# Performance work log

Measured on AMD Instinct MI355X. Metric: run time of the kernel, lower is better.

Reference implementation:

```python
import jax, jax.numpy as jnp
import numpy as np

N_NODES = 100000


def _gcn_norm(edge_src, edge_dst, n):
    ones = jnp.ones(edge_src.shape[0], dtype=jnp.float32)
    deg_out = jax.ops.segment_sum(ones, edge_src, num_segments=n)
    deg_in = jax.ops.segment_sum(ones, edge_dst, num_segments=n)
    norm_src = jax.lax.rsqrt(jnp.maximum(deg_out, 1.0))
    norm_dst = jax.lax.rsqrt(jnp.maximum(deg_in, 1.0))
    return norm_src, norm_dst


def _graph_conv(h, edge_src, edge_dst, norm_src, norm_dst, W, b, act):
    # symmetric-normalized aggregation: D^-1/2 A D^-1/2 h, then linear
    m = (h * norm_src[:, None])[edge_src]                       # [E, d] gather
    agg = jax.ops.segment_sum(m, edge_dst, num_segments=h.shape[0])  # [N, d] scatter-add
    agg = agg * norm_dst[:, None]
    out = agg @ W + b[: W.shape[1]]
    return act(out) if act is not None else out


def setup_inputs() -> dict:
    key = jax.random.key(0)
    ks = jax.random.split(key, 8)
    d_in, d_h, n_cls, E = 64, 64, 40, 1000000
    return {
        "features": jax.random.normal(ks[0], (N_NODES, d_in), dtype=jnp.float32),
        "edge_src": jax.random.randint(ks[1], (E,), 0, N_NODES),
        "edge_dst": jax.random.randint(ks[2], (E,), 0, N_NODES),
        "W1": jax.random.normal(ks[3], (d_in, d_h), dtype=jnp.float32) * (1.0 / np.sqrt(d_in)),
        "b1": jnp.zeros((d_h,), dtype=jnp.float32),
        "W2": jax.random.normal(ks[4], (d_h, d_h), dtype=jnp.float32) * (1.0 / np.sqrt(d_h)),
        "b2": jnp.zeros((d_h,), dtype=jnp.float32),
        "W3": jax.random.normal(ks[5], (d_h, n_cls), dtype=jnp.float32) * (1.0 / np.sqrt(d_h)),
        "b3": jnp.zeros((d_h,), dtype=jnp.float32),
    }


def reference(features, edge_src, edge_dst, W1, b1, W2, b2, W3, b3):
    norm_src, norm_dst = _gcn_norm(edge_src, edge_dst, features.shape[0])
    h = _graph_conv(features, edge_src, edge_dst, norm_src, norm_dst, W1, b1, jax.nn.relu)
    h = _graph_conv(h, edge_src, edge_dst, norm_src, norm_dst, W2, b2, jax.nn.relu)
    h = _graph_conv(h, edge_src, edge_dst, norm_src, norm_dst, W3, b3, None)
    return h
```

## Files before the change

kernel.cpp:

```cpp
#include <hip/hip_runtime.h>
#include <hip/hip_fp16.h>

#define D 64
#define THREADS 256
#define CAP 40
#define BSTRIDE 44

__global__ void init_kernel(int* __restrict__ cnt_out, int* __restrict__ buckets, int n) {
    int i = blockIdx.x * blockDim.x + threadIdx.x;
    if (i < n) {
        cnt_out[i] = 0;
        buckets[(size_t)i * BSTRIDE] = 0;
    }
}

__global__ void build_kernel(const int* __restrict__ src, const int* __restrict__ dst,
                             int* __restrict__ cnt_out, int* __restrict__ buckets, int E) {
    int base = (blockIdx.x * blockDim.x + threadIdx.x) * 4;
    if (base + 3 < E) {
        int4 s4 = *(const int4*)(src + base);
        int4 d4 = *(const int4*)(dst + base);
        atomicAdd(&cnt_out[s4.x], 1);
        atomicAdd(&cnt_out[s4.y], 1);
        atomicAdd(&cnt_out[s4.z], 1);
        atomicAdd(&cnt_out[s4.w], 1);
        int p0 = atomicAdd(&buckets[(size_t)d4.x * BSTRIDE], 1);
        int p1 = atomicAdd(&buckets[(size_t)d4.y * BSTRIDE], 1);
        int p2 = atomicAdd(&buckets[(size_t)d4.z * BSTRIDE], 1);
        int p3 = atomicAdd(&buckets[(size_t)d4.w * BSTRIDE], 1);
        if (p0 < CAP) buckets[(size_t)d4.x * BSTRIDE + 4 + p0] = s4.x;
        if (p1 < CAP) buckets[(size_t)d4.y * BSTRIDE + 4 + p1] = s4.y;
        if (p2 < CAP) buckets[(size_t)d4.z * BSTRIDE + 4 + p2] = s4.z;
        if (p3 < CAP) buckets[(size_t)d4.w * BSTRIDE + 4 + p3] = s4.w;
    } else {
        for (int i = base; i < E; ++i) {
            int s = src[i], d = dst[i];
            atomicAdd(&cnt_out[s], 1);
            int pos = atomicAdd(&buckets[(size_t)d * BSTRIDE], 1);
            if (pos < CAP) buckets[(size_t)d * BSTRIDE + 4 + pos] = s;
        }
    }
}

__global__ void prescale_kernel(const float* __restrict__ feat, const int* __restrict__ cnt_out,
                                __half* __restrict__ outp, int n16) {
    int i = blockIdx.x * blockDim.x + threadIdx.x;
    if (i < n16) {
        float s = rsqrtf(fmaxf((float)cnt_out[i >> 4], 1.0f));
        float4 v = ((const float4*)feat)[i];
        __half2 lo = __floats2half2_rn(v.x * s, v.y * s);
        __half2 hi = __floats2half2_rn(v.z * s, v.w * s);
        uint2 u;
        u.x = *(unsigned*)&lo;
        u.y = *(unsigned*)&hi;
        ((uint2*)outp)[i] = u;
    }
}

__device__ __forceinline__ float bcast(float v, int l) {
    return __uint_as_float(__builtin_amdgcn_readlane(__float_as_uint(v), l));
}

template <int DOUT, bool RELU, bool SOUT, bool OUT_HALF>
__global__ __launch_bounds__(THREADS)
void layer_kernel(const __half* __restrict__ h, const int* __restrict__ buckets,
                  const int* __restrict__ cnt_out,
                  const float* __restrict__ W, const float* __restrict__ b,
                  void* __restrict__ outv, int n) {
    const int t = threadIdx.x;
    const int wave = t >> 6;
    const int lane = t & 63;
    const int grp  = lane >> 4;
    const int c    = lane & 15;
    const int ln   = (lane < DOUT) ? lane : (DOUT - 1);

    float4 Wc[16];
#pragma unroll
    for (int k4 = 0; k4 < 16; ++k4) {
        Wc[k4].x = W[(4 * k4 + 0) * DOUT + ln];
        Wc[k4].y = W[(4 * k4 + 1) * DOUT + ln];
        Wc[k4].z = W[(4 * k4 + 2) * DOUT + ln];
        Wc[k4].w = W[(4 * k4 + 3) * DOUT + ln];
    }
    const float bl = b[ln];

    const int nquads = (n + 3) >> 2;
    for (int qd = blockIdx.x * 4 + wave; qd < nquads; qd += gridDim.x * 4) {
        int node0 = qd * 4;
        int node  = node0 + grp;
        bool valid = node < n;
        int node_c = valid ? node : 0;
        size_t bbase = (size_t)node_c * BSTRIDE;
        int dg = valid ? buckets[bbase] : 0;
        if (dg > CAP) dg = CAP;
        const int* epos = buckets + bbase + 4;

        float ax = 0.f, ay = 0.f, az = 0.f, aw = 0.f;
        float bx = 0.f, by = 0.f, bz = 0.f, bw = 0.f;

        int4 q0 = *(const int4*)(epos + 0);
        int4 q1 = *(const int4*)(epos + 4);
        int4 q2 = *(const int4*)(epos + 8);
        int4 q3 = *(const int4*)(epos + 12);
        int sidx[16];
        sidx[0]=q0.x; sidx[1]=q0.y; sidx[2]=q0.z; sidx[3]=q0.w;
        sidx[4]=q1.x; sidx[5]=q1.y; sidx[6]=q1.z; sidx[7]=q1.w;
        sidx[8]=q2.x; sidx[9]=q2.y; sidx[10]=q2.z; sidx[11]=q2.w;
        sidx[12]=q3.x; sidx[13]=q3.y; sidx[14]=q3.z; sidx[15]=q3.w;

        uint2 u[16];
#pragma unroll
        for (int j = 0; j < 16; ++j) {
            unsigned sj = (j < dg) ? (unsigned)sidx[j] : 0u;
            u[j] = *((const uint2*)(h + ((size_t)sj << 6)) + c);
        }
#pragma unroll
        for (int j = 0; j < 16; ++j) {
            float wj = (j < dg) ? 1.f : 0.f;
            float2 lo = __half22float2(*(__half2*)&u[j].x);
            float2 hi = __half22float2(*(__half2*)&u[j].y);
            if (j & 1) {
                ax = fmaf(lo.x, wj, ax); ay = fmaf(lo.y, wj, ay);
                az = fmaf(hi.x, wj, az); aw = fmaf(hi.y, wj, aw);
            } else {
                bx = fmaf(lo.x, wj, bx); by = fmaf(lo.y, wj, by);
                bz = fmaf(hi.x, wj, bz); bw = fmaf(hi.y, wj, bw);
            }
        }
        for (int e = 16; e < dg; e += 4) {
            int4 i4 = *(const int4*)(epos + e);
            int rem = dg - e;
            unsigned s0 = (unsigned)i4.x;
            unsigned s1 = (rem > 1) ? (unsigned)i4.y : 0u;
            unsigned s2 = (rem > 2) ? (unsigned)i4.z : 0u;
            unsigned s3 = (rem > 3) ? (unsigned)i4.w : 0u;
            float w1 = (rem > 1) ? 1.f : 0.f;
            float w2 = (rem > 2) ? 1.f : 0.f;
            float w3 = (rem > 3) ? 1.f : 0.f;
            uint2 u0 = *((const uint2*)(h + ((size_t)s0 << 6)) + c);
            uint2 u1 = *((const uint2*)(h + ((size_t)s1 << 6)) + c);
            uint2 u2 = *((const uint2*)(h + ((size_t)s2 << 6)) + c);
            uint2 u3 = *((const uint2*)(h + ((size_t)s3 << 6)) + c);
            float2 l0 = __half22float2(*(__half2*)&u0.x), h0 = __half22float2(*(__half2*)&u0.y);
            float2 l1 = __half22float2(*(__half2*)&u1.x), h1 = __half22float2(*(__half2*)&u1.y);
            float2 l2 = __half22float2(*(__half2*)&u2.x), h2 = __half22float2(*(__half2*)&u2.y);
            float2 l3 = __half22float2(*(__half2*)&u3.x), h3 = __half22float2(*(__half2*)&u3.y);
            ax += l0.x; ay += l0.y; az += h0.x; aw += h0.y;
            ax = fmaf(l1.x, w1, ax); ay = fmaf(l1.y, w1, ay);
            az = fmaf(h1.x, w1, az); aw = fmaf(h1.y, w1, aw);
            bx = fmaf(l2.x, w2, bx); by = fmaf(l2.y, w2, by);
            bz = fmaf(h2.x, w2, bz); bw = fmaf(h2.y, w2, bw);
            bx = fmaf(l3.x, w3, bx); by = fmaf(l3.y, w3, by);
            bz = fmaf(h3.x, w3, bz); bw = fmaf(h3.y, w3, bw);
        }
        ax += bx; ay += by; az += bz; aw += bw;

        float sA = 0.f, sB = 0.f, sC = 0.f, sD = 0.f;
#pragma unroll
        for (int cc = 0; cc < 16; ++cc) {
            sA = fmaf(bcast(ax,      cc), Wc[cc].x, sA);
            sB = fmaf(bcast(ax, 16 + cc), Wc[cc].x, sB);
            sC = fmaf(bcast(ax, 32 + cc), Wc[cc].x, sC);
            sD = fmaf(bcast(ax, 48 + cc), Wc[cc].x, sD);
            sA = fmaf(bcast(ay,      cc), Wc[cc].y, sA);
            sB = fmaf(bcast(ay, 16 + cc), Wc[cc].y, sB);
            sC = fmaf(bcast(ay, 32 + cc), Wc[cc].y, sC);
            sD = fmaf(bcast(ay, 48 + cc), Wc[cc].y, sD);
            sA = fmaf(bcast(az,      cc), Wc[cc].z, sA);
            sB = fmaf(bcast(az, 16 + cc), Wc[cc].z, sB);
            sC = fmaf(bcast(az, 32 + cc), Wc[cc].z, sC);
            sD = fmaf(bcast(az, 48 + cc), Wc[cc].z, sD);
            sA = fmaf(bcast(aw,      cc), Wc[cc].w, sA);
            sB = fmaf(bcast(aw, 16 + cc), Wc[cc].w, sB);
            sC = fmaf(bcast(aw, 32 + cc), Wc[cc].w, sC);
            sD = fmaf(bcast(aw, 48 + cc), Wc[cc].w, sD);
        }

        int dg0 = __builtin_amdgcn_readlane(dg, 0);
        int dg1 = __builtin_amdgcn_readlane(dg, 16);
        int dg2 = __builtin_amdgcn_readlane(dg, 32);
        int dg3 = __builtin_amdgcn_readlane(dg, 48);
        float nd0 = rsqrtf(fmaxf((float)dg0, 1.f));
        float nd1 = rsqrtf(fmaxf((float)dg1, 1.f));
        float nd2 = rsqrtf(fmaxf((float)dg2, 1.f));
        float nd3 = rsqrtf(fmaxf((float)dg3, 1.f));
        float ns0 = 1.f, ns1 = 1.f, ns2 = 1.f, ns3 = 1.f;
        if (SOUT) {
            ns0 = rsqrtf(fmaxf((float)cnt_out[node0], 1.f));
            ns1 = (node0 + 1 < n) ? rsqrtf(fmaxf((float)cnt_out[node0 + 1], 1.f)) : 0.f;
            ns2 = (node0 + 2 < n) ? rsqrtf(fmaxf((float)cnt_out[node0 + 2], 1.f)) : 0.f;
            ns3 = (node0 + 3 < n) ? rsqrtf(fmaxf((float)cnt_out[node0 + 3], 1.f)) : 0.f;
        }

        float o0 = fmaf(sA, nd0, bl);
        float o1 = fmaf(sB, nd1, bl);
        float o2 = fmaf(sC, nd2, bl);
        float o3 = fmaf(sD, nd3, bl);
        if (RELU) {
            o0 = fmaxf(o0, 0.f); o1 = fmaxf(o1, 0.f);
            o2 = fmaxf(o2, 0.f); o3 = fmaxf(o3, 0.f);
        }
        if (SOUT) { o0 *= ns0; o1 *= ns1; o2 *= ns2; o3 *= ns3; }
        if (lane < DOUT) {
            if (OUT_HALF) {
                __half* out = (__half*)outv;
                out[(size_t)node0 * DOUT + lane] = __float2half(o0);
                if (node0 + 1 < n) out[(size_t)(node0 + 1) * DOUT + lane] = __float2half(o1);
                if (node0 + 2 < n) out[(size_t)(node0 + 2) * DOUT + lane] = __float2half(o2);
                if (node0 + 3 < n) out[(size_t)(node0 + 3) * DOUT + lane] = __float2half(o3);
            } else {
                float* out = (float*)outv;
                out[(size_t)node0 * DOUT + lane] = o0;
                if (node0 + 1 < n) out[(size_t)(node0 + 1) * DOUT + lane] = o1;
                if (node0 + 2 < n) out[(size_t)(node0 + 2) * DOUT + lane] = o2;
                if (node0 + 3 < n) out[(size_t)(node0 + 3) * DOUT + lane] = o3;
            }
        }
    }
}

extern "C" void kernel_launch(void* const* d_in, const int* in_sizes, int n_in,
                              void* d_out, int out_size, void* d_ws, size_t ws_size,
                              hipStream_t stream) {
    const float* feat = (const float*)d_in[0];
    const int*   esrc = (const int*)d_in[1];
    const int*   edst = (const int*)d_in[2];
    const float* W1   = (const float*)d_in[3];
    const float* b1   = (const float*)d_in[4];
    const float* W2   = (const float*)d_in[5];
    const float* b2   = (const float*)d_in[6];
    const float* W3   = (const float*)d_in[7];
    const float* b3   = (const float*)d_in[8];
    float* out = (float*)d_out;

    const int E = in_sizes[1];
    const int N = in_sizes[0] / D;

    int* cnt_out = (int*)d_ws;
    int* buckets = cnt_out + N;
    __half* hA   = (__half*)(buckets + (size_t)N * BSTRIDE);
    __half* hB   = hA + (size_t)N * D;

    init_kernel<<<(N + THREADS - 1) / THREADS, THREADS, 0, stream>>>(cnt_out, buckets, N);

    const int ethreads4 = (E + 3) / 4;
    build_kernel<<<(ethreads4 + THREADS - 1) / THREADS, THREADS, 0, stream>>>(
        esrc, edst, cnt_out, buckets, E);

    const int n16 = N * (D / 4);
    prescale_kernel<<<(n16 + THREADS - 1) / THREADS, THREADS, 0, stream>>>(feat, cnt_out, hB, n16);

    const int lgrid = 2048;
    layer_kernel<D, true, true, true><<<lgrid, THREADS, 0, stream>>>(
        hB, buckets, cnt_out, W1, b1, hA, N);
    layer_kernel<D, true, true, true><<<lgrid, THREADS, 0, stream>>>(
        hA, buckets, cnt_out, W2, b2, hB, N);
    layer_kernel<40, false, false, false><<<lgrid, THREADS, 0, stream>>>(
        hB, buckets, cnt_out, W3, b3, out, N);
}
```

Measured before the change: 361.5 us.

## Process eight nodes per wave with 16-byte gathers and LDS-staged weights

The layer kernel now assigns 8 lanes per node (8 nodes per wave) and gathers each neighbor row with uint4 loads of 8 halves. The weight matrix moves from per-thread registers into shared memory, read per k inside the transform loop. The tail-edge loop becomes one edge per iteration, and the build kernel processes 2 edges per thread instead of 4. The goal is fewer gather instructions and more nodes in flight per wave, at the cost of more readlane broadcasts (8 per k) and LDS reads in the dense transform.

```diff
diff --git a/kernel.cpp b/kernel.cpp
--- a/kernel.cpp
+++ b/kernel.cpp
@@ -16,22 +16,16 @@
 
 __global__ void build_kernel(const int* __restrict__ src, const int* __restrict__ dst,
                              int* __restrict__ cnt_out, int* __restrict__ buckets, int E) {
-    int base = (blockIdx.x * blockDim.x + threadIdx.x) * 4;
-    if (base + 3 < E) {
-        int4 s4 = *(const int4*)(src + base);
-        int4 d4 = *(const int4*)(dst + base);
-        atomicAdd(&cnt_out[s4.x], 1);
-        atomicAdd(&cnt_out[s4.y], 1);
-        atomicAdd(&cnt_out[s4.z], 1);
-        atomicAdd(&cnt_out[s4.w], 1);
-        int p0 = atomicAdd(&buckets[(size_t)d4.x * BSTRIDE], 1);
-        int p1 = atomicAdd(&buckets[(size_t)d4.y * BSTRIDE], 1);
-        int p2 = atomicAdd(&buckets[(size_t)d4.z * BSTRIDE], 1);
-        int p3 = atomicAdd(&buckets[(size_t)d4.w * BSTRIDE], 1);
-        if (p0 < CAP) buckets[(size_t)d4.x * BSTRIDE + 4 + p0] = s4.x;
-        if (p1 < CAP) buckets[(size_t)d4.y * BSTRIDE + 4 + p1] = s4.y;
-        if (p2 < CAP) buckets[(size_t)d4.z * BSTRIDE + 4 + p2] = s4.z;
-        if (p3 < CAP) buckets[(size_t)d4.w * BSTRIDE + 4 + p3] = s4.w;
+    int base = (blockIdx.x * blockDim.x + threadIdx.x) * 2;
+    if (base + 1 < E) {
+        int2 s2 = *(const int2*)(src + base);
+        int2 d2 = *(const int2*)(dst + base);
+        atomicAdd(&cnt_out[s2.x], 1);
+        atomicAdd(&cnt_out[s2.y], 1);
+        int p0 = atomicAdd(&buckets[(size_t)d2.x * BSTRIDE], 1);
+        int p1 = atomicAdd(&buckets[(size_t)d2.y * BSTRIDE], 1);
+        if (p0 < CAP) buckets[(size_t)d2.x * BSTRIDE + 4 + p0] = s2.x;
+        if (p1 < CAP) buckets[(size_t)d2.y * BSTRIDE + 4 + p1] = s2.y;
     } else {
         for (int i = base; i < E; ++i) {
             int s = src[i], d = dst[i];
@@ -67,26 +61,21 @@
                   const int* __restrict__ cnt_out,
                   const float* __restrict__ W, const float* __restrict__ b,
                   void* __restrict__ outv, int n) {
+    __shared__ float Wl[D * DOUT];
     const int t = threadIdx.x;
+    for (int i = t; i < D * DOUT; i += THREADS) Wl[i] = W[i];
+    __syncthreads();
+
     const int wave = t >> 6;
     const int lane = t & 63;
-    const int grp  = lane >> 4;
-    const int c    = lane & 15;
+    const int grp  = lane >> 3;
+    const int c    = lane & 7;
     const int ln   = (lane < DOUT) ? lane : (DOUT - 1);
-
-    float4 Wc[16];
-#pragma unroll
-    for (int k4 = 0; k4 < 16; ++k4) {
-        Wc[k4].x = W[(4 * k4 + 0) * DOUT + ln];
-        Wc[k4].y = W[(4 * k4 + 1) * DOUT + ln];
-        Wc[k4].z = W[(4 * k4 + 2) * DOUT + ln];
-        Wc[k4].w = W[(4 * k4 + 3) * DOUT + ln];
-    }
     const float bl = b[ln];
 
-    const int nquads = (n + 3) >> 2;
-    for (int qd = blockIdx.x * 4 + wave; qd < nquads; qd += gridDim.x * 4) {
-        int node0 = qd * 4;
+    const int noctets = (n + 7) >> 3;
+    for (int oc = blockIdx.x * 4 + wave; oc < noctets; oc += gridDim.x * 4) {
+        int node0 = oc * 8;
         int node  = node0 + grp;
         bool valid = node < n;
         int node_c = valid ? node : 0;
@@ -94,9 +83,6 @@
         int dg = valid ? buckets[bbase] : 0;
         if (dg > CAP) dg = CAP;
         const int* epos = buckets + bbase + 4;
-
-        float ax = 0.f, ay = 0.f, az = 0.f, aw = 0.f;
-        float bx = 0.f, by = 0.f, bz = 0.f, bw = 0.f;
 
         int4 q0 = *(const int4*)(epos + 0);
         int4 q1 = *(const int4*)(epos + 4);
@@ -108,112 +94,61 @@
         sidx[8]=q2.x; sidx[9]=q2.y; sidx[10]=q2.z; sidx[11]=q2.w;
         sidx[12]=q3.x; sidx[13]=q3.y; sidx[14]=q3.z; sidx[15]=q3.w;
 
-        uint2 u[16];
+        uint4 u[16];
 #pragma unroll
         for (int j = 0; j < 16; ++j) {
             unsigned sj = (j < dg) ? (unsigned)sidx[j] : 0u;
-            u[j] = *((const uint2*)(h + ((size_t)sj << 6)) + c);
+            u[j] = *((const uint4*)(h + ((size_t)sj << 6)) + c);
         }
+
+        float a[8] = {0.f, 0.f, 0.f, 0.f, 0.f, 0.f, 0.f, 0.f};
 #pragma unroll
         for (int j = 0; j < 16; ++j) {
             float wj = (j < dg) ? 1.f : 0.f;
-            float2 lo = __half22float2(*(__half2*)&u[j].x);
-            float2 hi = __half22float2(*(__half2*)&u[j].y);
-            if (j & 1) {
-                ax = fmaf(lo.x, wj, ax); ay = fmaf(lo.y, wj, ay);
-                az = fmaf(hi.x, wj, az); aw = fmaf(hi.y, wj, aw);
-            } else {
-                bx = fmaf(lo.x, wj, bx); by = fmaf(lo.y, wj, by);
-                bz = fmaf(hi.x, wj, bz); bw = fmaf(hi.y, wj, bw);
+            const __half2* hp = reinterpret_cast<const __half2*>(&u[j]);
+            float2 f0 = __half22float2(hp[0]);
+            float2 f1 = __half22float2(hp[1]);
+            float2 f2 = __half22float2(hp[2]);
+            float2 f3 = __half22float2(hp[3]);
+            a[0] = fmaf(f0.x, wj, a[0]); a[1] = fmaf(f0.y, wj, a[1]);
+            a[2] = fmaf(f1.x, wj, a[2]); a[3] = fmaf(f1.y, wj, a[3]);
+            a[4] = fmaf(f2.x, wj, a[4]); a[5] = fmaf(f2.y, wj, a[5]);
+            a[6] = fmaf(f3.x, wj, a[6]); a[7] = fmaf(f3.y, wj, a[7]);
+        }
+        for (int e = 16; e < dg; ++e) {
+            unsigned sj = (unsigned)epos[e];
+            uint4 ue = *((const uint4*)(h + ((size_t)sj << 6)) + c);
+            const __half2* hp = reinterpret_cast<const __half2*>(&ue);
+            float2 f0 = __half22float2(hp[0]);
+            float2 f1 = __half22float2(hp[1]);
+            float2 f2 = __half22float2(hp[2]);
+            float2 f3 = __half22float2(hp[3]);
+            a[0] += f0.x; a[1] += f0.y; a[2] += f1.x; a[3] += f1.y;
+            a[4] += f2.x; a[5] += f2.y; a[6] += f3.x; a[7] += f3.y;
+        }
+
+        float s[8] = {0.f, 0.f, 0.f, 0.f, 0.f, 0.f, 0.f, 0.f};
+#pragma unroll
+        for (int k = 0; k < D; ++k) {
+            float wk = Wl[k * DOUT + ln];
+#pragma unroll
+            for (int g = 0; g < 8; ++g) {
+                s[g] = fmaf(bcast(a[k & 7], 8 * g + (k >> 3)), wk, s[g]);
             }
         }
-        for (int e = 16; e < dg; e += 4) {
-            int4 i4 = *(const int4*)(epos + e);
-            int rem = dg - e;
-            unsigned s0 = (unsigned)i4.x;
-            unsigned s1 = (rem > 1) ? (unsigned)i4.y : 0u;
-            unsigned s2 = (rem > 2) ? (unsigned)i4.z : 0u;
-            unsigned s3 = (rem > 3) ? (unsigned)i4.w : 0u;
-            float w1 = (rem > 1) ? 1.f : 0.f;
-            float w2 = (rem > 2) ? 1.f : 0.f;
-            float w3 = (rem > 3) ? 1.f : 0.f;
-            uint2 u0 = *((const uint2*)(h + ((size_t)s0 << 6)) + c);
-            uint2 u1 = *((const uint2*)(h + ((size_t)s1 << 6)) + c);
-            uint2 u2 = *((const uint2*)(h + ((size_t)s2 << 6)) + c);
-            uint2 u3 = *((const uint2*)(h + ((size_t)s3 << 6)) + c);
-            float2 l0 = __half22float2(*(__half2*)&u0.x), h0 = __half22float2(*(__half2*)&u0.y);
-            float2 l1 = __half22float2(*(__half2*)&u1.x), h1 = __half22float2(*(__half2*)&u1.y);
-            float2 l2 = __half22float2(*(__half2*)&u2.x), h2 = __half22float2(*(__half2*)&u2.y);
-            float2 l3 = __half22float2(*(__half2*)&u3.x), h3 = __half22float2(*(__half2*)&u3.y);
-            ax += l0.x; ay += l0.y; az += h0.x; aw += h0.y;
-            ax = fmaf(l1.x, w1, ax); ay = fmaf(l1.y, w1, ay);
-            az = fmaf(h1.x, w1, az); aw = fmaf(h1.y, w1, aw);
-            bx = fmaf(l2.x, w2, bx); by = fmaf(l2.y, w2, by);
-            bz = fmaf(h2.x, w2, bz); bw = fmaf(h2.y, w2, bw);
-            bx = fmaf(l3.x, w3, bx); by = fmaf(l3.y, w3, by);
-            bz = fmaf(h3.x, w3, bz); bw = fmaf(h3.y, w3, bw);
-        }
-        ax += bx; ay += by; az += bz; aw += bw;
 
-        float sA = 0.f, sB = 0.f, sC = 0.f, sD = 0.f;
 #pragma unroll
-        for (int cc = 0; cc < 16; ++cc) {
-            sA = fmaf(bcast(ax,      cc), Wc[cc].x, sA);
-            sB = fmaf(bcast(ax, 16 + cc), Wc[cc].x, sB);
-            sC = fmaf(bcast(ax, 32 + cc), Wc[cc].x, sC);
-            sD = fmaf(bcast(ax, 48 + cc), Wc[cc].x, sD);
-            sA = fmaf(bcast(ay,      cc), Wc[cc].y, sA);
-            sB = fmaf(bcast(ay, 16 + cc), Wc[cc].y, sB);
-            sC = fmaf(bcast(ay, 32 + cc), Wc[cc].y, sC);
-            sD = fmaf(bcast(ay, 48 + cc), Wc[cc].y, sD);
-            sA = fmaf(bcast(az,      cc), Wc[cc].z, sA);
-            sB = fmaf(bcast(az, 16 + cc), Wc[cc].z, sB);
-            sC = fmaf(bcast(az, 32 + cc), Wc[cc].z, sC);
-            sD = fmaf(bcast(az, 48 + cc), Wc[cc].z, sD);
-            sA = fmaf(bcast(aw,      cc), Wc[cc].w, sA);
-            sB = fmaf(bcast(aw, 16 + cc), Wc[cc].w, sB);
-            sC = fmaf(bcast(aw, 32 + cc), Wc[cc].w, sC);
-            sD = fmaf(bcast(aw, 48 + cc), Wc[cc].w, sD);
-        }
-
-        int dg0 = __builtin_amdgcn_readlane(dg, 0);
-        int dg1 = __builtin_amdgcn_readlane(dg, 16);
-        int dg2 = __builtin_amdgcn_readlane(dg, 32);
-        int dg3 = __builtin_amdgcn_readlane(dg, 48);
-        float nd0 = rsqrtf(fmaxf((float)dg0, 1.f));
-        float nd1 = rsqrtf(fmaxf((float)dg1, 1.f));
-        float nd2 = rsqrtf(fmaxf((float)dg2, 1.f));
-        float nd3 = rsqrtf(fmaxf((float)dg3, 1.f));
-        float ns0 = 1.f, ns1 = 1.f, ns2 = 1.f, ns3 = 1.f;
-        if (SOUT) {
-            ns0 = rsqrtf(fmaxf((float)cnt_out[node0], 1.f));
-            ns1 = (node0 + 1 < n) ? rsqrtf(fmaxf((float)cnt_out[node0 + 1], 1.f)) : 0.f;
-            ns2 = (node0 + 2 < n) ? rsqrtf(fmaxf((float)cnt_out[node0 + 2], 1.f)) : 0.f;
-            ns3 = (node0 + 3 < n) ? rsqrtf(fmaxf((float)cnt_out[node0 + 3], 1.f)) : 0.f;
-        }
-
-        float o0 = fmaf(sA, nd0, bl);
-        float o1 = fmaf(sB, nd1, bl);
-        float o2 = fmaf(sC, nd2, bl);
-        float o3 = fmaf(sD, nd3, bl);
-        if (RELU) {
-            o0 = fmaxf(o0, 0.f); o1 = fmaxf(o1, 0.f);
-            o2 = fmaxf(o2, 0.f); o3 = fmaxf(o3, 0.f);
-        }
-        if (SOUT) { o0 *= ns0; o1 *= ns1; o2 *= ns2; o3 *= ns3; }
-        if (lane < DOUT) {
-            if (OUT_HALF) {
-                __half* out = (__half*)outv;
-                out[(size_t)node0 * DOUT + lane] = __float2half(o0);
-                if (node0 + 1 < n) out[(size_t)(node0 + 1) * DOUT + lane] = __float2half(o1);
-                if (node0 + 2 < n) out[(size_t)(node0 + 2) * DOUT + lane] = __float2half(o2);
-                if (node0 + 3 < n) out[(size_t)(node0 + 3) * DOUT + lane] = __float2half(o3);
-            } else {
-                float* out = (float*)outv;
-                out[(size_t)node0 * DOUT + lane] = o0;
-                if (node0 + 1 < n) out[(size_t)(node0 + 1) * DOUT + lane] = o1;
-                if (node0 + 2 < n) out[(size_t)(node0 + 2) * DOUT + lane] = o2;
-                if (node0 + 3 < n) out[(size_t)(node0 + 3) * DOUT + lane] = o3;
+        for (int g = 0; g < 8; ++g) {
+            int ng = node0 + g;
+            if (ng >= n) continue;
+            int dgg = __builtin_amdgcn_readlane(dg, 8 * g);
+            float nd = rsqrtf(fmaxf((float)dgg, 1.f));
+            float o = fmaf(s[g], nd, bl);
+            if (RELU) o = fmaxf(o, 0.f);
+            if (SOUT) o *= rsqrtf(fmaxf((float)cnt_out[ng], 1.f));
+            if (lane < DOUT) {
+                if (OUT_HALF) ((__half*)outv)[(size_t)ng * DOUT + lane] = __float2half(o);
+                else          ((float*)outv)[(size_t)ng * DOUT + lane] = o;
             }
         }
     }
@@ -243,8 +178,8 @@
 
     init_kernel<<<(N + THREADS - 1) / THREADS, THREADS, 0, stream>>>(cnt_out, buckets, N);
 
-    const int ethreads4 = (E + 3) / 4;
-    build_kernel<<<(ethreads4 + THREADS - 1) / THREADS, THREADS, 0, stream>>>(
+    const int ethreads2 = (E + 1) / 2;
+    build_kernel<<<(ethreads2 + THREADS - 1) / THREADS, THREADS, 0, stream>>>(
         esrc, edst, cnt_out, buckets, E);
 
     const int n16 = N * (D / 4);
```

After: 379.4 us. 5.0% more time.
